# Kernel optimization log

Measured on AMD Instinct MI355X. Metric: run time of the kernel, lower is better.

## Reference

```python
import jax, jax.numpy as jnp
import numpy as np

EPS = 1e-5  # torch LayerNorm default


def _ln(x, w, b):
    m = jnp.mean(x, axis=-1, keepdims=True)
    v = jnp.mean((x - m) ** 2, axis=-1, keepdims=True)
    return (x - m) / jnp.sqrt(v + EPS) * w + b


def _conv1x1(x, w, b):
    # x: [B,C,H,W], w: [O,C], b: [O]
    return jnp.einsum('bchw,oc->bohw', x, w) + b[None, :, None, None]


def setup_inputs() -> dict:
    key = jax.random.key(0)
    ks = jax.random.split(key, 5)
    B, Cin, H, W = 8, 384, 64, 64
    D, N = 128, 512
    s = lambda k, shape, scale=0.02: jax.random.normal(k, shape, jnp.float32) * scale
    return {
        'x': jax.random.normal(ks[0], (B, Cin, H, W), jnp.float32),
        'DR': jax.random.normal(ks[1], (N, D), jnp.float32),
        'conv_in_w': s(ks[2], (D, Cin)),
        'conv_in_b': jnp.zeros((D,), jnp.float32),
        'sem_w': s(ks[3], (D, D)),
        'sem_b': jnp.zeros((D,), jnp.float32),
        'norm1_w': jnp.ones((D,), jnp.float32),
        'norm1_b': jnp.zeros((D,), jnp.float32),
        'norm2_w': jnp.ones((D,), jnp.float32),
        'norm2_b': jnp.zeros((D,), jnp.float32),
        'conv_out_w': s(ks[4], (Cin, D)),
        'conv_out_b': jnp.zeros((Cin,), jnp.float32),
    }


def reference(x, DR, conv_in_w, conv_in_b, sem_w, sem_b, norm1_w, norm1_b,
              norm2_w, norm2_b, conv_out_w, conv_out_b):
    B, _, H, W = x.shape
    N = DR.shape[0]
    x_align = _conv1x1(x, conv_in_w, conv_in_b)                      # [B,D,H,W]
    x_sem = _conv1x1(x_align, sem_w, sem_b)                          # semantic_extra (1x1 conv)
    x_sem = x_sem.transpose(0, 2, 3, 1).reshape(B, H * W, -1)        # [B,HW,D]
    x_sem = _ln(x_sem, norm1_w, norm1_b)
    dr = _ln(DR, norm2_w, norm2_b).T                                 # [D,N] (same for all batches)
    # NOTE: original applies norm_1 TWICE for the numerator (faithful quirk)
    c_u = jnp.einsum('bld,dn->bln', _ln(x_sem, norm1_w, norm1_b), dr)  # [B,HW,N]
    c_d_l = jnp.sqrt(jnp.sum(x_sem ** 2, axis=-1, keepdims=True))      # [B,HW,1]
    c_d_r = jnp.sqrt(jnp.sum(dr ** 2, axis=0, keepdims=True))[None]    # [1,1,N]
    sim = c_u / (c_d_l * c_d_r)
    sim_soft = jax.nn.softmax(sim, axis=-1)                          # [B,HW,N]
    sim2d = sim_soft.transpose(0, 2, 1).reshape(B, N, H, W)
    degrad = jnp.einsum('bln,dn->bdl', sim_soft, dr).reshape(B, -1, H, W)  # [B,D,H,W]
    # pow-mask with per-batch min-max normalization
    mask_v = jnp.max(sim2d ** 3, axis=1, keepdims=True)              # [B,1,H,W]
    mn = jnp.min(mask_v.reshape(B, -1), axis=1).reshape(B, 1, 1, 1)
    mx = jnp.max(mask_v.reshape(B, -1), axis=1).reshape(B, 1, 1, 1)
    mask_v = 1.0 - (mask_v - mn) / (mx - mn)
    # topk row selection (torch fancy indexing gives [B,B,K,N]; squeeze(1) is a no-op for B>1)
    max_values = jnp.max(sim_soft, axis=2)                           # [B,HW]
    K = (H * W) // 50
    _, top_idx = jax.lax.top_k(max_values, K)                        # [B,K]
    results = jnp.take(sim_soft, top_idx, axis=1)                    # [B,B,K,N]
    out_img = _conv1x1(degrad, conv_out_w, conv_out_b)               # [B,Cin,H,W]
    return (mask_v, out_img, results)
```

## Files before the change

### kernel.cpp

```cpp
#include <hip/hip_runtime.h>
#include <cstdint>

#define EPS 1e-5f
#define BB   8
#define CIN  384
#define HWs  4096
#define LT   32768
#define DD   128
#define NN   512
#define TOPK 81

typedef short short8 __attribute__((ext_vector_type(8)));
typedef float f32x4  __attribute__((ext_vector_type(4)));

__device__ __forceinline__ unsigned short f2bf(float x) {
  unsigned u = __float_as_uint(x);
  u += 0x7fffu + ((u >> 16) & 1u);
  return (unsigned short)(u >> 16);
}
__device__ __forceinline__ float bf2f(unsigned u16) {
  return __uint_as_float(u16 << 16);
}
__device__ __forceinline__ void put_frag(unsigned short* buf, int tile, int rc, int k, float v) {
  int ks = k >> 5, g = (k >> 3) & 3, j = k & 7;
  int basehw = ((tile * 4 + ks) * 2) * 512 + (g * 16 + rc) * 8 + j;
  unsigned short hi = f2bf(v);
  buf[basehw] = hi;
  buf[basehw + 512] = f2bf(v - bf2f(hi));
}

__global__ __launch_bounds__(64) void k_dr(const float* __restrict__ DR,
    const float* __restrict__ w2, const float* __restrict__ b2,
    const float* __restrict__ w1, const float* __restrict__ b1,
    unsigned short* __restrict__ drwF, unsigned short* __restrict__ drlnF,
    float* __restrict__ t2, float* __restrict__ rcr) {
  int n = blockIdx.x;
  int lane = threadIdx.x;
  const float* row = DR + n * DD;
  float x0 = row[lane], x1 = row[lane + 64];
  float s = x0 + x1, sq = x0 * x0 + x1 * x1;
  #pragma unroll
  for (int o = 32; o; o >>= 1) { s += __shfl_xor(s, o); sq += __shfl_xor(sq, o); }
  float m = s * (1.f / 128.f);
  float v = sq * (1.f / 128.f) - m * m;
  float inv = rsqrtf(v + EPS);
  float y0 = (x0 - m) * inv * w2[lane] + b2[lane];
  float y1 = (x1 - m) * inv * w2[lane + 64] + b2[lane + 64];
  int nt = n >> 4, cc = n & 15;
  put_frag(drwF, nt, cc, lane, y0 * w1[lane]);
  put_frag(drwF, nt, cc, lane + 64, y1 * w1[lane + 64]);
  int ks = n >> 5, gB = (n >> 3) & 3, j = n & 7;
  {
    int d = lane;
    unsigned short hi = f2bf(y0);
    int base = (((d >> 4) * 16 + ks) * 2) * 512 + (gB * 16 + (d & 15)) * 8 + j;
    drlnF[base] = hi;
    drlnF[base + 512] = f2bf(y0 - bf2f(hi));
  }
  {
    int d = lane + 64;
    unsigned short hi = f2bf(y1);
    int base = (((d >> 4) * 16 + ks) * 2) * 512 + (gB * 16 + (d & 15)) * 8 + j;
    drlnF[base] = hi;
    drlnF[base + 512] = f2bf(y1 - bf2f(hi));
  }
  float pt2 = y0 * b1[lane] + y1 * b1[lane + 64];
  float pss = y0 * y0 + y1 * y1;
  #pragma unroll
  for (int o = 32; o; o >>= 1) { pt2 += __shfl_xor(pt2, o); pss += __shfl_xor(pss, o); }
  if (lane == 0) { t2[n] = pt2; rcr[n] = rsqrtf(pss); }
}

__global__ __launch_bounds__(256) void k_bprep(const float* __restrict__ src,
                                               unsigned short* __restrict__ dst,
                                               int K) {
  int rt = blockIdx.x, kb = blockIdx.y;
  int t = threadIdx.x, m = t >> 4, kg = t & 15;
  int k0 = kb * 128 + kg * 8;
  const float* s = src + (size_t)(rt * 16 + m) * K + k0;
  float4 f0 = *(const float4*)s;
  float4 f1 = *(const float4*)(s + 4);
  float vs[8] = {f0.x, f0.y, f0.z, f0.w, f1.x, f1.y, f1.z, f1.w};
  short8 hi, lo;
  #pragma unroll
  for (int j = 0; j < 8; ++j) {
    unsigned short h = f2bf(vs[j]);
    hi[j] = (short)h;
    lo[j] = (short)f2bf(vs[j] - bf2f(h));
  }
  int nkt = K >> 5;
  int ks = k0 >> 5, g = (k0 >> 3) & 3;
  short8* D8 = (short8*)dst;
  int base = ((rt * nkt + ks) * 2) * 64 + g * 16 + m;
  D8[base] = hi;
  D8[base + 64] = lo;
}

__global__ __launch_bounds__(256) void k_convin(const float* __restrict__ x,
    const unsigned short* __restrict__ WinF, const float* __restrict__ bias,
    unsigned short* __restrict__ xaF) {
  __shared__ float smem[64 * 132];
  int t = threadIdx.x;
  int w = t >> 6, lane = t & 63, m = lane & 15, g = lane >> 4;
  int l0 = blockIdx.x * 64;
  int b = l0 >> 12, hw0 = l0 & 4095;
  const float* xb = x + (size_t)b * CIN * HWs + hw0;
  const short8* B8 = (const short8*)WinF;
  f32x4 acc[4][2];
  #pragma unroll
  for (int lt = 0; lt < 4; ++lt)
    #pragma unroll
    for (int j2 = 0; j2 < 2; ++j2) acc[lt][j2] = (f32x4){0.f, 0.f, 0.f, 0.f};
  for (int ks = 0; ks < 12; ++ks) {
    short8 ah[4], al[4];
    const float* xc = xb + (size_t)(ks * 32 + g * 8) * HWs;
    #pragma unroll
    for (int lt = 0; lt < 4; ++lt) {
      const float* xcl = xc + lt * 16 + m;
      float v[8];
      #pragma unroll
      for (int j = 0; j < 8; ++j) v[j] = xcl[(size_t)j * HWs];
      #pragma unroll
      for (int j = 0; j < 8; ++j) {
        unsigned short h = f2bf(v[j]);
        ah[lt][j] = (short)h;
        al[lt][j] = (short)f2bf(v[j] - bf2f(h));
      }
    }
    #pragma unroll
    for (int j2 = 0; j2 < 2; ++j2) {
      int dt = w * 2 + j2;
      short8 bh = B8[((dt * 12 + ks) * 2 + 0) * 64 + lane];
      short8 bl = B8[((dt * 12 + ks) * 2 + 1) * 64 + lane];
      #pragma unroll
      for (int lt = 0; lt < 4; ++lt) {
        acc[lt][j2] = __builtin_amdgcn_mfma_f32_16x16x32_bf16(ah[lt], bh, acc[lt][j2], 0, 0, 0);
        acc[lt][j2] = __builtin_amdgcn_mfma_f32_16x16x32_bf16(ah[lt], bl, acc[lt][j2], 0, 0, 0);
        acc[lt][j2] = __builtin_amdgcn_mfma_f32_16x16x32_bf16(al[lt], bh, acc[lt][j2], 0, 0, 0);
      }
    }
  }
  float bia[2] = {bias[w * 32 + m], bias[w * 32 + 16 + m]};
  #pragma unroll
  for (int lt = 0; lt < 4; ++lt)
    #pragma unroll
    for (int j2 = 0; j2 < 2; ++j2)
      #pragma unroll
      for (int r = 0; r < 4; ++r)
        smem[(lt * 16 + g * 4 + r) * 132 + (w * 2 + j2) * 16 + m] = acc[lt][j2][r] + bia[j2];
  __syncthreads();
  short8* X8 = (short8*)xaF;
  #pragma unroll
  for (int it = 0; it < 4; ++it) {
    int idx = it * 256 + t;
    int l = idx & 63, dq = idx >> 6;
    const float* src = &smem[l * 132 + dq * 8];
    float4 f0 = *(const float4*)src;
    float4 f1 = *(const float4*)(src + 4);
    float vs[8] = {f0.x, f0.y, f0.z, f0.w, f1.x, f1.y, f1.z, f1.w};
    short8 hi, lo;
    #pragma unroll
    for (int j = 0; j < 8; ++j) {
      unsigned short h = f2bf(vs[j]);
      hi[j] = (short)h;
      lo[j] = (short)f2bf(vs[j] - bf2f(h));
    }
    int ltg = (l0 + l) >> 4;
    int idx8 = ((ltg * 4 + (dq >> 2)) * 2) * 64 + (dq & 3) * 16 + (l & 15);
    X8[idx8] = hi;
    X8[idx8 + 64] = lo;
  }
}

__global__ __launch_bounds__(256) void k_sem(const unsigned short* __restrict__ xaF,
    const unsigned short* __restrict__ semWF, const float* __restrict__ bias,
    const float* __restrict__ w1, const float* __restrict__ b1,
    unsigned short* __restrict__ ApF, float* __restrict__ rclv) {
  __shared__ float smem[64 * 132];
  __shared__ float sredS[64][4], sredQ[64][4];
  __shared__ float rowM[64], rowI[64];
  int t = threadIdx.x;
  int w = t >> 6, lane = t & 63, m = lane & 15, g = lane >> 4;
  int l0 = blockIdx.x * 64;
  int lt0 = l0 >> 4;
  const short8* A8 = (const short8*)xaF;
  const short8* B8 = (const short8*)semWF;
  f32x4 acc[4][2];
  #pragma unroll
  for (int lt = 0; lt < 4; ++lt)
    #pragma unroll
    for (int j2 = 0; j2 < 2; ++j2) acc[lt][j2] = (f32x4){0.f, 0.f, 0.f, 0.f};
  #pragma unroll
  for (int ks = 0; ks < 4; ++ks) {
    short8 ah[4], al[4];
    #pragma unroll
    for (int lt = 0; lt < 4; ++lt) {
      ah[lt] = A8[(((lt0 + lt) * 4 + ks) * 2 + 0) * 64 + lane];
      al[lt] = A8[(((lt0 + lt) * 4 + ks) * 2 + 1) * 64 + lane];
    }
    #pragma unroll
    for (int j2 = 0; j2 < 2; ++j2) {
      int dt = w * 2 + j2;
      short8 bh = B8[((dt * 4 + ks) * 2 + 0) * 64 + lane];
      short8 bl = B8[((dt * 4 + ks) * 2 + 1) * 64 + lane];
      #pragma unroll
      for (int lt = 0; lt < 4; ++lt) {
        acc[lt][j2] = __builtin_amdgcn_mfma_f32_16x16x32_bf16(ah[lt], bh, acc[lt][j2], 0, 0, 0);
        acc[lt][j2] = __builtin_amdgcn_mfma_f32_16x16x32_bf16(ah[lt], bl, acc[lt][j2], 0, 0, 0);
        acc[lt][j2] = __builtin_amdgcn_mfma_f32_16x16x32_bf16(al[lt], bh, acc[lt][j2], 0, 0, 0);
      }
    }
  }
  float bia[2] = {bias[w * 32 + m], bias[w * 32 + 16 + m]};
  #pragma unroll
  for (int lt = 0; lt < 4; ++lt)
    #pragma unroll
    for (int j2 = 0; j2 < 2; ++j2)
      #pragma unroll
      for (int r = 0; r < 4; ++r) acc[lt][j2][r] += bia[j2];
  float s1[4][4], q1[4][4];
  #pragma unroll
  for (int lt = 0; lt < 4; ++lt)
    #pragma unroll
    for (int r = 0; r < 4; ++r) {
      float a = acc[lt][0][r], b2v = acc[lt][1][r];
      s1[lt][r] = a + b2v;
      q1[lt][r] = a * a + b2v * b2v;
    }
  #pragma unroll
  for (int o = 1; o < 16; o <<= 1)
    #pragma unroll
    for (int lt = 0; lt < 4; ++lt)
      #pragma unroll
      for (int r = 0; r < 4; ++r) {
        s1[lt][r] += __shfl_xor(s1[lt][r], o);
        q1[lt][r] += __shfl_xor(q1[lt][r], o);
      }
  if (m == 0) {
    #pragma unroll
    for (int lt = 0; lt < 4; ++lt)
      #pragma unroll
      for (int r = 0; r < 4; ++r) {
        sredS[lt * 16 + g * 4 + r][w] = s1[lt][r];
        sredQ[lt * 16 + g * 4 + r][w] = q1[lt][r];
      }
  }
  __syncthreads();
  if (t < 64) {
    float S = sredS[t][0] + sredS[t][1] + sredS[t][2] + sredS[t][3];
    float Q = sredQ[t][0] + sredQ[t][1] + sredQ[t][2] + sredQ[t][3];
    float mu = S * (1.f / 128.f);
    float var = Q * (1.f / 128.f) - mu * mu;
    rowM[t] = mu;
    rowI[t] = rsqrtf(var + EPS);
  }
  __syncthreads();
  float w1v[2] = {w1[w * 32 + m], w1[w * 32 + 16 + m]};
  float b1v[2] = {b1[w * 32 + m], b1[w * 32 + 16 + m]};
  #pragma unroll
  for (int lt = 0; lt < 4; ++lt)
    #pragma unroll
    for (int r = 0; r < 4; ++r) {
      float mu = rowM[lt * 16 + g * 4 + r];
      float iv = rowI[lt * 16 + g * 4 + r];
      float y0 = (acc[lt][0][r] - mu) * iv * w1v[0] + b1v[0];
      float y1 = (acc[lt][1][r] - mu) * iv * w1v[1] + b1v[1];
      acc[lt][0][r] = y0; acc[lt][1][r] = y1;
      s1[lt][r] = y0 + y1;
      q1[lt][r] = y0 * y0 + y1 * y1;
    }
  #pragma unroll
  for (int o = 1; o < 16; o <<= 1)
    #pragma unroll
    for (int lt = 0; lt < 4; ++lt)
      #pragma unroll
      for (int r = 0; r < 4; ++r) {
        s1[lt][r] += __shfl_xor(s1[lt][r], o);
        q1[lt][r] += __shfl_xor(q1[lt][r], o);
      }
  if (m == 0) {
    #pragma unroll
    for (int lt = 0; lt < 4; ++lt)
      #pragma unroll
      for (int r = 0; r < 4; ++r) {
        sredS[lt * 16 + g * 4 + r][w] = s1[lt][r];
        sredQ[lt * 16 + g * 4 + r][w] = q1[lt][r];
      }
  }
  __syncthreads();
  if (t < 64) {
    float S = sredS[t][0] + sredS[t][1] + sredS[t][2] + sredS[t][3];
    float Q = sredQ[t][0] + sredQ[t][1] + sredQ[t][2] + sredQ[t][3];
    float m2 = S * (1.f / 128.f);
    float v2 = Q * (1.f / 128.f) - m2 * m2;
    float inv2 = rsqrtf(v2 + EPS);
    float rcl = rsqrtf(Q);
    rowM[t] = m2;
    rowI[t] = inv2 * rcl;
    rclv[l0 + t] = rcl;
  }
  __syncthreads();
  #pragma unroll
  for (int lt = 0; lt < 4; ++lt)
    #pragma unroll
    for (int r = 0; r < 4; ++r) {
      float m2 = rowM[lt * 16 + g * 4 + r];
      float sc = rowI[lt * 16 + g * 4 + r];
      smem[(lt * 16 + g * 4 + r) * 132 + w * 32 + m] = (acc[lt][0][r] - m2) * sc;
      smem[(lt * 16 + g * 4 + r) * 132 + w * 32 + 16 + m] = (acc[lt][1][r] - m2) * sc;
    }
  __syncthreads();
  short8* O8 = (short8*)ApF;
  #pragma unroll
  for (int it = 0; it < 4; ++it) {
    int idx = it * 256 + t;
    int l = idx & 63, dq = idx >> 6;
    const float* src = &smem[l * 132 + dq * 8];
    float4 f0 = *(const float4*)src;
    float4 f1 = *(const float4*)(src + 4);
    float vs[8] = {f0.x, f0.y, f0.z, f0.w, f1.x, f1.y, f1.z, f1.w};
    short8 hi, lo;
    #pragma unroll
    for (int j = 0; j < 8; ++j) {
      unsigned short h = f2bf(vs[j]);
      hi[j] = (short)h;
      lo[j] = (short)f2bf(vs[j] - bf2f(h));
    }
    int ltg = (l0 + l) >> 4;
    int idx8 = ((ltg * 4 + (dq >> 2)) * 2) * 64 + (dq & 3) * 16 + (l & 15);
    O8[idx8] = hi;
    O8[idx8 + 64] = lo;
  }
}

__global__ __launch_bounds__(256) void k_scores(const unsigned short* __restrict__ ApF,
    const unsigned short* __restrict__ drwF, const float* __restrict__ t2g,
    const float* __restrict__ rcrg, const float* __restrict__ rclg,
    unsigned short* __restrict__ pF, float* __restrict__ maxv) {
  __shared__ float sred[32][5];
  int t = threadIdx.x;
  int w = t >> 6, lane = t & 63, c = lane & 15, g = lane >> 4;
  int l0 = blockIdx.x * 32;
  int lt0 = blockIdx.x * 2;
  const short8* A8 = (const short8*)ApF;
  const short8* B8 = (const short8*)drwF;
  f32x4 acc[2][8];
  #pragma unroll
  for (int il = 0; il < 2; ++il)
    #pragma unroll
    for (int jn = 0; jn < 8; ++jn) acc[il][jn] = (f32x4){0.f, 0.f, 0.f, 0.f};
  #pragma unroll
  for (int ks = 0; ks < 4; ++ks) {
    short8 ah0 = A8[((lt0 * 4 + ks) * 2 + 0) * 64 + lane];
    short8 al0 = A8[((lt0 * 4 + ks) * 2 + 1) * 64 + lane];
    short8 ah1 = A8[(((lt0 + 1) * 4 + ks) * 2 + 0) * 64 + lane];
    short8 al1 = A8[(((lt0 + 1) * 4 + ks) * 2 + 1) * 64 + lane];
    #pragma unroll
    for (int jn = 0; jn < 8; ++jn) {
      int nt = w * 8 + jn;
      short8 bh = B8[((nt * 4 + ks) * 2 + 0) * 64 + lane];
      short8 bl = B8[((nt * 4 + ks) * 2 + 1) * 64 + lane];
      acc[0][jn] = __builtin_amdgcn_mfma_f32_16x16x32_bf16(ah0, bh, acc[0][jn], 0, 0, 0);
      acc[0][jn] = __builtin_amdgcn_mfma_f32_16x16x32_bf16(ah0, bl, acc[0][jn], 0, 0, 0);
      acc[0][jn] = __builtin_amdgcn_mfma_f32_16x16x32_bf16(al0, bh, acc[0][jn], 0, 0, 0);
      acc[1][jn] = __builtin_amdgcn_mfma_f32_16x16x32_bf16(ah1, bh, acc[1][jn], 0, 0, 0);
      acc[1][jn] = __builtin_amdgcn_mfma_f32_16x16x32_bf16(ah1, bl, acc[1][jn], 0, 0, 0);
      acc[1][jn] = __builtin_amdgcn_mfma_f32_16x16x32_bf16(al1, bh, acc[1][jn], 0, 0, 0);
    }
  }
  float rcrv[8], t2v[8];
  #pragma unroll
  for (int jn = 0; jn < 8; ++jn) {
    int n = w * 128 + jn * 16 + c;
    rcrv[jn] = rcrg[n]; t2v[jn] = t2g[n];
  }
  float rclr[2][4];
  #pragma unroll
  for (int il = 0; il < 2; ++il)
    #pragma unroll
    for (int r = 0; r < 4; ++r)
      rclr[il][r] = rclg[l0 + il * 16 + g * 4 + r];
  float M[2][4];
  #pragma unroll
  for (int il = 0; il < 2; ++il)
    #pragma unroll
    for (int r = 0; r < 4; ++r) M[il][r] = -1e30f;
  #pragma unroll
  for (int il = 0; il < 2; ++il)
    #pragma unroll
    for (int jn = 0; jn < 8; ++jn) {
      f32x4 a = acc[il][jn];
      #pragma unroll
      for (int r = 0; r < 4; ++r) {
        float s = rcrv[jn] * (a[r] + rclr[il][r] * t2v[jn]);
        a[r] = s;
        M[il][r] = fmaxf(M[il][r], s);
      }
      acc[il][jn] = a;
    }
  #pragma unroll
  for (int o = 1; o < 16; o <<= 1)
    #pragma unroll
    for (int il = 0; il < 2; ++il)
      #pragma unroll
      for (int r = 0; r < 4; ++r)
        M[il][r] = fmaxf(M[il][r], __shfl_xor(M[il][r], o));
  if (c == 0) {
    #pragma unroll
    for (int il = 0; il < 2; ++il)
      #pragma unroll
      for (int r = 0; r < 4; ++r)
        sred[il * 16 + g * 4 + r][w] = M[il][r];
  }
  __syncthreads();
  if (t < 32) {
    float mm = fmaxf(fmaxf(sred[t][0], sred[t][1]), fmaxf(sred[t][2], sred[t][3]));
    sred[t][4] = mm;
  }
  __syncthreads();
  float Mf[2][4];
  #pragma unroll
  for (int il = 0; il < 2; ++il)
    #pragma unroll
    for (int r = 0; r < 4; ++r)
      Mf[il][r] = sred[il * 16 + g * 4 + r][4];
  float S[2][4];
  #pragma unroll
  for (int il = 0; il < 2; ++il)
    #pragma unroll
    for (int r = 0; r < 4; ++r) S[il][r] = 0.f;
  #pragma unroll
  for (int il = 0; il < 2; ++il)
    #pragma unroll
    for (int jn = 0; jn < 8; ++jn) {
      f32x4 a = acc[il][jn];
      #pragma unroll
      for (int r = 0; r < 4; ++r) {
        float e = expf(a[r] - Mf[il][r]);
        a[r] = e;
        S[il][r] += e;
      }
      acc[il][jn] = a;
    }
  #pragma unroll
  for (int o = 1; o < 16; o <<= 1)
    #pragma unroll
    for (int il = 0; il < 2; ++il)
      #pragma unroll
      for (int r = 0; r < 4; ++r)
        S[il][r] += __shfl_xor(S[il][r], o);
  __syncthreads();
  if (c == 0) {
    #pragma unroll
    for (int il = 0; il < 2; ++il)
      #pragma unroll
      for (int r = 0; r < 4; ++r)
        sred[il * 16 + g * 4 + r][w] = S[il][r];
  }
  __syncthreads();
  if (t < 32) {
    float tot = sred[t][0] + sred[t][1] + sred[t][2] + sred[t][3];
    float rs = 1.f / tot;
    sred[t][4] = rs;
    maxv[l0 + t] = rs;
  }
  __syncthreads();
  #pragma unroll
  for (int il = 0; il < 2; ++il) {
    int lt = lt0 + il;
    #pragma unroll
    for (int r = 0; r < 4; ++r) {
      int mrow = g * 4 + r;
      float rs = sred[il * 16 + mrow][4];
      #pragma unroll
      for (int jn = 0; jn < 8; ++jn) {
        int ks = w * 4 + (jn >> 1);
        int gB = (jn * 2 + (c >> 3)) & 3;
        pF[((lt * 16 + ks) * 64 + gB * 16 + mrow) * 8 + (c & 7)] =
            f2bf(acc[il][jn][r] * rs);
      }
    }
  }
}

__global__ __launch_bounds__(256) void k_deg(const unsigned short* __restrict__ pF,
    const unsigned short* __restrict__ drlnF, const unsigned short* __restrict__ WoF,
    const float* __restrict__ bo, float* __restrict__ out_img) {
  __shared__ float smem[64 * 132];
  int t = threadIdx.x;
  int w = t >> 6, lane = t & 63, c = lane & 15, g = lane >> 4;
  int l0 = blockIdx.x * 64;
  int lt0 = l0 >> 4;
  const short8* P8 = (const short8*)pF;
  const short8* D8 = (const short8*)drlnF;
  const short8* W8 = (const short8*)WoF;
  f32x4 acc[4][2];
  #pragma unroll
  for (int lt = 0; lt < 4; ++lt)
    #pragma unroll
    for (int j2 = 0; j2 < 2; ++j2) acc[lt][j2] = (f32x4){0.f, 0.f, 0.f, 0.f};
  for (int ks = 0; ks < 16; ++ks) {
    short8 a0 = P8[((lt0 + 0) * 16 + ks) * 64 + lane];
    short8 a1 = P8[((lt0 + 1) * 16 + ks) * 64 + lane];
    short8 a2 = P8[((lt0 + 2) * 16 + ks) * 64 + lane];
    short8 a3 = P8[((lt0 + 3) * 16 + ks) * 64 + lane];
    #pragma unroll
    for (int j2 = 0; j2 < 2; ++j2) {
      int dt = w * 2 + j2;
      short8 bh = D8[((dt * 16 + ks) * 2 + 0) * 64 + lane];
      short8 bl = D8[((dt * 16 + ks) * 2 + 1) * 64 + lane];
      acc[0][j2] = __builtin_amdgcn_mfma_f32_16x16x32_bf16(a0, bh, acc[0][j2], 0, 0, 0);
      acc[0][j2] = __builtin_amdgcn_mfma_f32_16x16x32_bf16(a0, bl, acc[0][j2], 0, 0, 0);
      acc[1][j2] = __builtin_amdgcn_mfma_f32_16x16x32_bf16(a1, bh, acc[1][j2], 0, 0, 0);
      acc[1][j2] = __builtin_amdgcn_mfma_f32_16x16x32_bf16(a1, bl, acc[1][j2], 0, 0, 0);
      acc[2][j2] = __builtin_amdgcn_mfma_f32_16x16x32_bf16(a2, bh, acc[2][j2], 0, 0, 0);
      acc[2][j2] = __builtin_amdgcn_mfma_f32_16x16x32_bf16(a2, bl, acc[2][j2], 0, 0, 0);
      acc[3][j2] = __builtin_amdgcn_mfma_f32_16x16x32_bf16(a3, bh, acc[3][j2], 0, 0, 0);
      acc[3][j2] = __builtin_amdgcn_mfma_f32_16x16x32_bf16(a3, bl, acc[3][j2], 0, 0, 0);
    }
  }
  #pragma unroll
  for (int lt = 0; lt < 4; ++lt)
    #pragma unroll
    for (int j2 = 0; j2 < 2; ++j2)
      #pragma unroll
      for (int r = 0; r < 4; ++r)
        smem[(lt * 16 + g * 4 + r) * 132 + w * 32 + j2 * 16 + c] = acc[lt][j2][r];
  __syncthreads();
  f32x4 acc2[4][6];
  #pragma unroll
  for (int lt = 0; lt < 4; ++lt)
    #pragma unroll
    for (int ot = 0; ot < 6; ++ot) acc2[lt][ot] = (f32x4){0.f, 0.f, 0.f, 0.f};
  #pragma unroll
  for (int ks2 = 0; ks2 < 4; ++ks2) {
    short8 dh[4];
    #pragma unroll
    for (int lt = 0; lt < 4; ++lt) {
      const float* src = &smem[(lt * 16 + c) * 132 + ks2 * 32 + g * 8];
      float4 f0 = *(const float4*)src;
      float4 f1 = *(const float4*)(src + 4);
      float vs[8] = {f0.x, f0.y, f0.z, f0.w, f1.x, f1.y, f1.z, f1.w};
      #pragma unroll
      for (int j = 0; j < 8; ++j) dh[lt][j] = (short)f2bf(vs[j]);
    }
    #pragma unroll
    for (int ot = 0; ot < 6; ++ot) {
      int otg = w * 6 + ot;
      short8 wh = W8[((otg * 4 + ks2) * 2 + 0) * 64 + lane];
      short8 wl = W8[((otg * 4 + ks2) * 2 + 1) * 64 + lane];
      #pragma unroll
      for (int lt = 0; lt < 4; ++lt) {
        acc2[lt][ot] = __builtin_amdgcn_mfma_f32_16x16x32_bf16(dh[lt], wh, acc2[lt][ot], 0, 0, 0);
        acc2[lt][ot] = __builtin_amdgcn_mfma_f32_16x16x32_bf16(dh[lt], wl, acc2[lt][ot], 0, 0, 0);
      }
    }
  }
  __syncthreads();
  int b = l0 >> 12, hw0 = l0 & 4095;
  float* ob = out_img + (size_t)b * CIN * HWs + hw0;
  float bov[6];
  #pragma unroll
  for (int ot = 0; ot < 6; ++ot) bov[ot] = bo[w * 96 + ot * 16 + c];
  for (int ot = 0; ot < 6; ++ot) {
    #pragma unroll
    for (int lt = 0; lt < 4; ++lt)
      #pragma unroll
      for (int r = 0; r < 4; ++r)
        smem[(lt * 16 + g * 4 + r) * 65 + w * 16 + c] = acc2[lt][ot][r] + bov[ot];
    __syncthreads();
    #pragma unroll
    for (int i = 0; i < 16; ++i) {
      int idx = t + i * 256;
      int o_l = idx >> 6, ll = idx & 63;
      int o = (o_l >> 4) * 96 + ot * 16 + (o_l & 15);
      ob[(size_t)o * HWs + ll] = smem[ll * 65 + o_l];
    }
    __syncthreads();
  }
}

__global__ __launch_bounds__(256) void k_mask(const float* __restrict__ maxv,
                                              float* __restrict__ outm) {
  int b = blockIdx.x, t = threadIdx.x;
  float c[16];
  float mn = 1e30f, mx = -1e30f;
  #pragma unroll
  for (int j = 0; j < 16; ++j) {
    float x = maxv[b * HWs + t + j * 256];
    float cc = x * x * x;
    c[j] = cc;
    mn = fminf(mn, cc); mx = fmaxf(mx, cc);
  }
  #pragma unroll
  for (int o = 32; o; o >>= 1) { mn = fminf(mn, __shfl_xor(mn, o)); mx = fmaxf(mx, __shfl_xor(mx, o)); }
  __shared__ float smn[4], smx[4];
  int w = t >> 6;
  if ((t & 63) == 0) { smn[w] = mn; smx[w] = mx; }
  __syncthreads();
  mn = fminf(fminf(smn[0], smn[1]), fminf(smn[2], smn[3]));
  mx = fmaxf(fmaxf(smx[0], smx[1]), fmaxf(smx[2], smx[3]));
  float sc = 1.f / (mx - mn);
  #pragma unroll
  for (int j = 0; j < 16; ++j)
    outm[b * HWs + t + j * 256] = 1.f - (c[j] - mn) * sc;
}

__global__ __launch_bounds__(256) void k_topk(const float* __restrict__ maxv,
                                              int* __restrict__ tix) {
  __shared__ unsigned int hist[4][256];
  __shared__ unsigned long long slist[TOPK];
  __shared__ unsigned long long bc_prefix;
  __shared__ int bc_need, scount;
  int b = blockIdx.x, t = threadIdx.x;
  int w = t >> 6;
  unsigned long long key[16];
  #pragma unroll
  for (int j = 0; j < 16; ++j) {
    int idx = t + j * 256;
    unsigned int bits = __float_as_uint(maxv[b * HWs + idx]);
    key[j] = ((unsigned long long)bits << 12) | (unsigned)(4095 - idx);
  }
  if (t == 0) { bc_prefix = 0ull; bc_need = TOPK; scount = 0; }
  for (int r = 0; r < 6; ++r) {
    int shift = 40 - 8 * r;
    unsigned int* hflat = (unsigned int*)hist;
    hflat[t] = 0; hflat[t + 256] = 0; hflat[t + 512] = 0; hflat[t + 768] = 0;
    __syncthreads();
    unsigned long long prefix = bc_prefix;
    int bins[16];
    #pragma unroll
    for (int j = 0; j < 16; ++j)
      bins[j] = ((key[j] >> (shift + 8)) == prefix) ? (int)((key[j] >> shift) & 255) : -1;
    #pragma unroll
    for (int j = 0; j < 16; ++j) {
      if (bins[j] >= 0) {
        int cnt = 1;
        #pragma unroll
        for (int j2 = j + 1; j2 < 16; ++j2)
          if (bins[j2] == bins[j]) { bins[j2] = -1; ++cnt; }
        atomicAdd(&hist[w][bins[j]], (unsigned)cnt);
      }
    }
    __syncthreads();
    if (t < 64) {
      int cb[4], s = 0;
      #pragma unroll
      for (int j = 0; j < 4; ++j) {
        int bin = 255 - (t * 4 + j);
        cb[j] = (int)(hist[0][bin] + hist[1][bin] + hist[2][bin] + hist[3][bin]);
        s += cb[j];
      }
      int P = s;
      #pragma unroll
      for (int o = 1; o < 64; o <<= 1) {
        int u = __shfl_up(P, o);
        if (t >= o) P += u;
      }
      int need = bc_need;
      unsigned long long mask = __ballot(P >= need);
      int first = __ffsll((long long)mask) - 1;
      if (t == first) {
        int acc = P - s;
        #pragma unroll
        for (int j = 0; j < 4; ++j) {
          if (acc + cb[j] >= need) {
            bc_prefix = (prefix << 8) | (unsigned)(255 - (t * 4 + j));
            bc_need = need - acc;
            break;
          }
          acc += cb[j];
        }
      }
    }
    __syncthreads();
  }
  unsigned long long K81 = bc_prefix;
  #pragma unroll
  for (int j = 0; j < 16; ++j)
    if (key[j] >= K81) {
      int pos = atomicAdd(&scount, 1);
      slist[pos] = key[j];
    }
  __syncthreads();
  if (t < TOPK) {
    unsigned long long mine = slist[t];
    int rank = 0;
    for (int i = 0; i < TOPK; ++i) rank += (slist[i] > mine) ? 1 : 0;
    tix[b * TOPK + rank] = 4095 - (int)(mine & 0xFFFull);
  }
}

__global__ __launch_bounds__(128) void k_gather(const unsigned short* __restrict__ pF,
    const int* __restrict__ tix, float* __restrict__ outr) {
  int gB_ = blockIdx.x;
  int k = gB_ % TOPK;
  int bb = gB_ / TOPK;
  int b2 = bb & 7, b = bb >> 3;
  int l = b * HWs + tix[b2 * TOPK + k];
  int lt = l >> 4, mrow = l & 15;
  int t = threadIdx.x;
  int ks = t >> 3, gq = (t >> 1) & 3, j0 = (t & 1) * 4;
  int base = ((lt * 16 + ks) * 64 + gq * 16 + mrow) * 8 + j0;
  const unsigned* src = (const unsigned*)(pF + base);
  unsigned u0 = src[0], u1 = src[1];
  float4 v = {bf2f(u0 & 0xffffu), bf2f(u0 >> 16), bf2f(u1 & 0xffffu), bf2f(u1 >> 16)};
  *(float4*)(outr + (size_t)gB_ * NN + t * 4) = v;
}

extern "C" void kernel_launch(void* const* d_in, const int* in_sizes, int n_in,
                              void* d_out, int out_size, void* d_ws, size_t ws_size,
                              hipStream_t stream) {
  const float* x    = (const float*)d_in[0];
  const float* DR   = (const float*)d_in[1];
  const float* win  = (const float*)d_in[2];
  const float* bin  = (const float*)d_in[3];
  const float* sw   = (const float*)d_in[4];
  const float* sb   = (const float*)d_in[5];
  const float* n1w  = (const float*)d_in[6];
  const float* n1b  = (const float*)d_in[7];
  const float* n2w  = (const float*)d_in[8];
  const float* n2b  = (const float*)d_in[9];
  const float* wout = (const float*)d_in[10];
  const float* bout = (const float*)d_in[11];
  float* out = (float*)d_out;
  float* W = (float*)d_ws;

  unsigned short* drwF  = (unsigned short*)(W);
  float* t2   = W + 65536;
  float* rcr  = W + 66048;
  float* rclv = W + 66560;
  float* maxv = W + 99328;
  unsigned short* drlnF = (unsigned short*)(W + 132096);
  unsigned short* WoF   = (unsigned short*)(W + 197632);
  unsigned short* WinF  = (unsigned short*)(W + 246784);
  unsigned short* semWF = (unsigned short*)(W + 295936);
  unsigned short* ApF   = (unsigned short*)(W + 312320);
  unsigned short* xaF   = (unsigned short*)(W + 4506624);
  unsigned short* pF    = (unsigned short*)(W + 4506624);
  int*   tix  = (int*)(W + 12895232);

  float* out_mask = out;
  float* out_img  = out + 32768;
  float* out_res  = out + 32768 + 12582912;

  k_dr    <<<NN, 64, 0, stream>>>(DR, n2w, n2b, n1w, n1b, drwF, drlnF, t2, rcr);
  k_bprep <<<dim3(8, 3),  256, 0, stream>>>(win,  WinF,  CIN);
  k_bprep <<<dim3(8, 1),  256, 0, stream>>>(sw,   semWF, DD);
  k_bprep <<<dim3(24, 1), 256, 0, stream>>>(wout, WoF,   DD);
  k_convin<<<512,  256, 0, stream>>>(x, WinF, bin, xaF);
  k_sem   <<<512,  256, 0, stream>>>(xaF, semWF, sb, n1w, n1b, ApF, rclv);
  k_scores<<<1024, 256, 0, stream>>>(ApF, drwF, t2, rcr, rclv, pF, maxv);
  k_deg   <<<512,  256, 0, stream>>>(pF, drlnF, WoF, bout, out_img);
  k_mask  <<<BB,   256, 0, stream>>>(maxv, out_mask);
  k_topk  <<<BB,   256, 0, stream>>>(maxv, tix);
  k_gather<<<BB * BB * TOPK, 128, 0, stream>>>(pF, tix, out_res);
}
```

Measured before the change: 251.6 us.

## Stage softmax probabilities in LDS for 16-byte coalesced stores in k_scores

The scores kernel now writes normalized bf16 probabilities into a padded shared-memory tile and then stores them to global memory as 16-byte short8 vectors, replacing scattered 2-byte stores. The row max and sum reductions are done redundantly by every thread with a vector LDS read, which removes two barriers. expf is replaced with __expf. This adds about 33KB of LDS per block, which may reduce occupancy, and uses a less precise exponential.

```diff
diff --git a/kernel.cpp b/kernel.cpp
--- a/kernel.cpp
+++ b/kernel.cpp
@@ -337,7 +337,9 @@
     const unsigned short* __restrict__ drwF, const float* __restrict__ t2g,
     const float* __restrict__ rcrg, const float* __restrict__ rclg,
     unsigned short* __restrict__ pF, float* __restrict__ maxv) {
-  __shared__ float sred[32][5];
+  __shared__ __align__(16) float sredM[32][4];
+  __shared__ __align__(16) float sredS[32][4];
+  __shared__ __align__(16) unsigned short plds[32 * 520];
   int t = threadIdx.x;
   int w = t >> 6, lane = t & 63, c = lane & 15, g = lane >> 4;
   int l0 = blockIdx.x * 32;
@@ -410,20 +412,17 @@
     for (int il = 0; il < 2; ++il)
       #pragma unroll
       for (int r = 0; r < 4; ++r)
-        sred[il * 16 + g * 4 + r][w] = M[il][r];
-  }
-  __syncthreads();
-  if (t < 32) {
-    float mm = fmaxf(fmaxf(sred[t][0], sred[t][1]), fmaxf(sred[t][2], sred[t][3]));
-    sred[t][4] = mm;
+        sredM[il * 16 + g * 4 + r][w] = M[il][r];
   }
   __syncthreads();
   float Mf[2][4];
   #pragma unroll
   for (int il = 0; il < 2; ++il)
     #pragma unroll
-    for (int r = 0; r < 4; ++r)
-      Mf[il][r] = sred[il * 16 + g * 4 + r][4];
+    for (int r = 0; r < 4; ++r) {
+      f32x4 mv = *(const f32x4*)(&sredM[il * 16 + g * 4 + r][0]);
+      Mf[il][r] = fmaxf(fmaxf(mv[0], mv[1]), fmaxf(mv[2], mv[3]));
+    }
   float S[2][4];
   #pragma unroll
   for (int il = 0; il < 2; ++il)
@@ -436,7 +435,7 @@
       f32x4 a = acc[il][jn];
       #pragma unroll
       for (int r = 0; r < 4; ++r) {
-        float e = expf(a[r] - Mf[il][r]);
+        float e = __expf(a[r] - Mf[il][r]);
         a[r] = e;
         S[il][r] += e;
       }
@@ -449,37 +448,51 @@
       #pragma unroll
       for (int r = 0; r < 4; ++r)
         S[il][r] += __shfl_xor(S[il][r], o);
-  __syncthreads();
   if (c == 0) {
     #pragma unroll
     for (int il = 0; il < 2; ++il)
       #pragma unroll
       for (int r = 0; r < 4; ++r)
-        sred[il * 16 + g * 4 + r][w] = S[il][r];
-  }
-  __syncthreads();
-  if (t < 32) {
-    float tot = sred[t][0] + sred[t][1] + sred[t][2] + sred[t][3];
-    float rs = 1.f / tot;
-    sred[t][4] = rs;
-    maxv[l0 + t] = rs;
-  }
-  __syncthreads();
-  #pragma unroll
-  for (int il = 0; il < 2; ++il) {
-    int lt = lt0 + il;
+        sredS[il * 16 + g * 4 + r][w] = S[il][r];
+  }
+  __syncthreads();
+  float RS[2][4];
+  #pragma unroll
+  for (int il = 0; il < 2; ++il)
     #pragma unroll
     for (int r = 0; r < 4; ++r) {
-      int mrow = g * 4 + r;
-      float rs = sred[il * 16 + mrow][4];
-      #pragma unroll
-      for (int jn = 0; jn < 8; ++jn) {
-        int ks = w * 4 + (jn >> 1);
-        int gB = (jn * 2 + (c >> 3)) & 3;
-        pF[((lt * 16 + ks) * 64 + gB * 16 + mrow) * 8 + (c & 7)] =
-            f2bf(acc[il][jn][r] * rs);
-      }
-    }
+      f32x4 sv = *(const f32x4*)(&sredS[il * 16 + g * 4 + r][0]);
+      float tot = sv[0] + sv[1] + sv[2] + sv[3];
+      RS[il][r] = 1.f / tot;
+    }
+  if (w == 0 && c == 0) {
+    #pragma unroll
+    for (int il = 0; il < 2; ++il)
+      #pragma unroll
+      for (int r = 0; r < 4; ++r)
+        maxv[l0 + il * 16 + g * 4 + r] = RS[il][r];
+  }
+  #pragma unroll
+  for (int il = 0; il < 2; ++il)
+    #pragma unroll
+    for (int jn = 0; jn < 8; ++jn)
+      #pragma unroll
+      for (int r = 0; r < 4; ++r)
+        plds[(il * 16 + g * 4 + r) * 520 + w * 128 + jn * 16 + c] =
+            f2bf(acc[il][jn][r] * RS[il][r]);
+  __syncthreads();
+  short8* P8o = (short8*)pF;
+  #pragma unroll
+  for (int it = 0; it < 8; ++it) {
+    int slot = it * 256 + t;
+    int ltl = slot >> 10;
+    int ks = (slot >> 6) & 15;
+    int gB = (slot >> 4) & 3;
+    int mrow = slot & 15;
+    int row = ltl * 16 + mrow;
+    int n0 = ks * 32 + gB * 8;
+    short8 v = *(const short8*)(&plds[row * 520 + n0]);
+    P8o[blockIdx.x * 2048 + slot] = v;
   }
 }
 
```

New measurement: 242.5 us. 3.6% less time.
